# Kernel optimization log

Hardware: AMD Instinct MI355X
Metric: run time of the kernel (lower is better)

The kernel has to match this reference:

```python
import jax, jax.numpy as jnp
import numpy as np

NUM_EXPERTS = 8


def setup_inputs() -> dict:
    key = jax.random.key(0)
    k1, k2, k3 = jax.random.split(key, 3)
    M, K, E, N, TOPK = 16384, 1024, NUM_EXPERTS, 2048, 2
    local_hidden_states = jax.random.normal(k1, (M, K), dtype=jnp.float32)
    up_weight = jax.random.normal(k2, (E, K, N), dtype=jnp.float32) * 0.02
    full_topk_ids = jax.random.randint(k3, (M, TOPK), 0, E, dtype=jnp.int64)
    return {
        "local_hidden_states": local_hidden_states,
        "up_weight": up_weight,
        "full_topk_ids": full_topk_ids,
    }


def reference(local_hidden_states, up_weight, full_topk_ids):
    # WORLD_SIZE == 1 -> all-gather is the identity; full token set == local shard.
    full_hidden = local_hidden_states                     # [M, K]
    M, K = full_hidden.shape
    E, _, N = up_weight.shape
    topk = full_topk_ids.shape[1]

    # Each token is routed to `topk` experts: replicate rows, flatten routing ids.
    h_rep = jnp.repeat(full_hidden, topk, axis=0)         # [M*topk, K]
    flat_ids = full_topk_ids.reshape(-1)                  # [M*topk]

    # Expert-grouped GEMM: out[p] = h_rep[p] @ up_weight[flat_ids[p]].
    # Loop over the small fixed expert count, masking rows (dense reference
    # for the irregular grouped GEMM; avoids a [M*topk, K, N] weight gather).
    inter = jnp.zeros((M * topk, N), dtype=full_hidden.dtype)
    for e in range(E):
        mask = (flat_ids == e).astype(full_hidden.dtype)[:, None]   # [M*topk, 1]
        inter = inter + (h_rep @ up_weight[e]) * mask                # [M*topk, N]

    # Fused gated SiLU: split the fused gate/up projection in half.
    half = N // 2
    gate, up = inter[:, :half], inter[:, half:]
    return jax.nn.silu(gate) * up                          # [M*topk, N//2]
```

## Files before the change

### kernel.cpp

```cpp
#include <hip/hip_runtime.h>
#include <hip/hip_bf16.h>
#include <stdint.h>

typedef __attribute__((ext_vector_type(4))) float f32x4;
typedef __attribute__((ext_vector_type(8))) short bf16x8;
typedef __attribute__((ext_vector_type(4))) float float4v;

static constexpr int KD    = 1024;
static constexpr int ND    = 2048;
static constexpr int NE    = 8;
static constexpr int MROWS = 16384;
static constexpr int RFLAT = 32768;
static constexpr int OUTN  = 1024;

static constexpr size_t WS_ROWLIST = 1024;
static constexpr size_t WS_HB      = 262144;
static constexpr size_t WS_WT      = 262144 + (size_t)33554432;

__device__ __forceinline__ unsigned short f2bf(float f) {
  uint32_t u = __float_as_uint(f);
  uint32_t r = (u + 0x7FFFu + ((u >> 16) & 1u)) >> 16;
  return (unsigned short)r;
}

__device__ __forceinline__ void gload16(const void* g, void* l) {
  __builtin_amdgcn_global_load_lds(
      (__attribute__((address_space(1))) void*)(void*)g,
      (__attribute__((address_space(3))) void*)l, 16, 0, 0);
}

__global__ void k_detect(const int* __restrict__ ids32, int* __restrict__ wsi) {
  int t = blockIdx.x * 256 + threadIdx.x;
  int i = 2 * t + 1;
  if (i < RFLAT && ids32[i] != 0) atomicOr(&wsi[31], 1);
}

__device__ __forceinline__ int read_id(const int* ids32, int t, int mode) {
  return (mode ? ids32[t] : ids32[2 * t]) & 7;
}

__global__ void k_count(const int* __restrict__ ids, int* __restrict__ wsi) {
  __shared__ int h[8];
  const int tid = threadIdx.x;
  if (tid < 8) h[tid] = 0;
  __syncthreads();
  const int mode = wsi[31];
  const int base = blockIdx.x * 512 + tid;
  atomicAdd(&h[read_id(ids, base, mode)], 1);
  atomicAdd(&h[read_id(ids, base + 256, mode)], 1);
  __syncthreads();
  if (tid < 8 && h[tid]) atomicAdd(&wsi[tid], h[tid]);
}

__global__ void k_scan(int* wsi) {
  if (threadIdx.x == 0) {
    int o = 0, to = 0;
    for (int e = 0; e < NE; ++e) {
      int c = wsi[e];
      wsi[16 + e] = o;
      wsi[8 + e]  = o;
      wsi[40 + e] = to;
      o += c;
      to += (c + 255) / 256;
    }
    wsi[16 + NE] = o;
    wsi[40 + NE] = to;
  }
}

__global__ void k_scatter(const int* __restrict__ ids, int* __restrict__ wsi,
                          int* __restrict__ rowlist) {
  __shared__ int h[8], base[8], c2[8];
  const int tid = threadIdx.x;
  if (tid < 8) { h[tid] = 0; c2[tid] = 0; }
  __syncthreads();
  const int mode = wsi[31];
  const int t = blockIdx.x * 256 + tid;
  const int e = read_id(ids, t, mode);
  atomicAdd(&h[e], 1);
  __syncthreads();
  if (tid < 8 && h[tid]) base[tid] = atomicAdd(&wsi[8 + tid], h[tid]);
  __syncthreads();
  const int r = atomicAdd(&c2[e], 1);
  rowlist[base[e] + r] = t;
}

__global__ void k_cvtH(const float* __restrict__ H, unsigned short* __restrict__ Hb) {
  const int n4 = (MROWS * KD) / 4;
  const int stride = gridDim.x * blockDim.x;
  for (int i = blockIdx.x * blockDim.x + threadIdx.x; i < n4; i += stride) {
    float4v v = ((const float4v*)H)[i];
    ushort4 o;
    o.x = f2bf(v.x); o.y = f2bf(v.y); o.z = f2bf(v.z); o.w = f2bf(v.w);
    ((ushort4*)Hb)[i] = o;
  }
}

__global__ void k_cvtW(const float* __restrict__ W, unsigned short* __restrict__ Wt) {
  __shared__ float tile[64][65];
  const int e  = blockIdx.z;
  const int n0 = blockIdx.x * 64;
  const int k0 = blockIdx.y * 64;
  const int tx = threadIdx.x, ty = threadIdx.y;
  const float* Wp = W + (size_t)e * KD * ND;
  #pragma unroll
  for (int i = ty; i < 64; i += 8)
    tile[i][tx] = Wp[(size_t)(k0 + i) * ND + n0 + tx];
  __syncthreads();
  unsigned short* Wo = Wt + (size_t)e * ND * KD;
  #pragma unroll
  for (int i = ty; i < 64; i += 8)
    Wo[(size_t)(n0 + i) * KD + k0 + tx] = f2bf(tile[tx][i]);
}

__global__ __launch_bounds__(512, 2) void k_gemm(
    const unsigned short* __restrict__ Hb, const unsigned short* __restrict__ Wt,
    const int* __restrict__ wsi, const int* __restrict__ rowlist,
    float* __restrict__ Out) {
  const int bid = blockIdx.x;
  const int xcd = bid & 7;
  const int j   = bid >> 3;
  const int colblk = j & 7;
  const int rt  = xcd + (j >> 3) * 8;
  if (rt >= wsi[48]) return;
  int e = 0;
  #pragma unroll
  for (int q = 1; q < 8; ++q)
    if (rt >= wsi[40 + q]) e = q;
  const int cnt = wsi[e];
  const int tile_base = (rt - wsi[40 + e]) * 256;
  const int tile_cnt = min(256, cnt - tile_base);
  const int off = wsi[16 + e] + tile_base;
  const int c0 = colblk * 128;

  __shared__ char lds[131072];
  __shared__ int s_rows[256];

  const int t = threadIdx.x;
  if (t < 256) s_rows[t] = rowlist[off + min(t, tile_cnt - 1)];
  __syncthreads();

  const int srow = t >> 2;
  const int coff = ((t & 3) ^ ((t >> 3) & 3)) * 16;
  const char* sA0 = (const char*)Hb + (size_t)(s_rows[srow] >> 1) * (KD * 2) + coff;
  const char* sA1 = (const char*)Hb + (size_t)(s_rows[128 + srow] >> 1) * (KD * 2) + coff;
  auto wcol_of = [&](int jc) {
    const int wn_s = jc >> 6, r64 = jc & 63;
    const int h_s = r64 >> 4, l_s = r64 & 15;
    return (h_s < 2) ? (c0 + wn_s * 32 + h_s * 16 + l_s)
                     : (OUTN + c0 + wn_s * 32 + (h_s - 2) * 16 + l_s);
  };
  const char* sB0 = (const char*)Wt + ((size_t)e * ND + wcol_of(srow)) * (KD * 2) + coff;
  const char* sB1 = (const char*)Wt + ((size_t)e * ND + wcol_of(128 + srow)) * (KD * 2) + coff;

  const int lane = t & 63, wid = t >> 6;
  const int wm = wid >> 2, wn = wid & 3;
  const int kc = lane >> 4, l15 = lane & 15;

  f32x4 acc[8][4];
  #pragma unroll
  for (int m = 0; m < 8; ++m)
    #pragma unroll
    for (int h = 0; h < 4; ++h)
      acc[m][h] = (f32x4){0.f, 0.f, 0.f, 0.f};

  int aoff[2][8], boff[2][4];
  #pragma unroll
  for (int q = 0; q < 2; ++q) {
    #pragma unroll
    for (int m = 0; m < 8; ++m) {
      const int r = wm * 128 + m * 16 + l15;
      aoff[q][m] = q * 16384 + r * 64 + ((kc ^ ((r >> 1) & 3)) * 16);
    }
    #pragma unroll
    for (int h = 0; h < 4; ++h) {
      const int jb = wn * 64 + h * 16 + l15;
      boff[q][h] = 32768 + q * 16384 + jb * 64 + ((kc ^ ((jb >> 1) & 3)) * 16);
    }
  }

  auto SA = [&](int kt, int q, char* buf) {
    const int go = kt * 128 + q * 64;
    gload16(sA0 + go, buf + q * 16384 + t * 16);
    gload16(sA1 + go, buf + q * 16384 + 8192 + t * 16);
  };
  auto SB = [&](int kt, int q, char* buf) {
    const int go = kt * 128 + q * 64;
    gload16(sB0 + go, buf + 32768 + q * 16384 + t * 16);
    gload16(sB1 + go, buf + 32768 + q * 16384 + 8192 + t * 16);
  };

  bf16x8 af[4], bfv[4];
  auto LDA = [&](const char* cb, int q, int mlo) {
    #pragma unroll
    for (int m = 0; m < 4; ++m) af[m] = *(const bf16x8*)(cb + aoff[q][mlo + m]);
  };
  auto LDB = [&](const char* cb, int q) {
    #pragma unroll
    for (int h = 0; h < 4; ++h) bfv[h] = *(const bf16x8*)(cb + boff[q][h]);
  };
  auto MM = [&](int mlo) {
    __builtin_amdgcn_s_setprio(1);
    #pragma unroll
    for (int m = 0; m < 4; ++m)
      #pragma unroll
      for (int h = 0; h < 4; ++h)
        acc[mlo + m][h] =
            __builtin_amdgcn_mfma_f32_16x16x32_bf16(af[m], bfv[h], acc[mlo + m][h], 0, 0, 0);
    __builtin_amdgcn_s_setprio(0);
  };
#define GUARD4 asm volatile("s_waitcnt vmcnt(4)" ::: "memory")
#define GUARD0 asm volatile("s_waitcnt vmcnt(0)" ::: "memory")
#define BAR __builtin_amdgcn_s_barrier()

  SA(0, 0, lds); SB(0, 0, lds); SA(0, 1, lds); SB(0, 1, lds);
  GUARD4; BAR;

  for (int k = 0; k < 15; ++k) {
    const char* cb = lds + (k & 1) * 65536;
    char* nb = lds + ((k + 1) & 1) * 65536;
    LDA(cb, 0, 0); LDB(cb, 0);
    SA(k + 1, 0, nb);
    BAR; MM(0); BAR;
    LDA(cb, 0, 4);
    SB(k + 1, 0, nb);
    GUARD4; BAR; MM(4); BAR;
    LDA(cb, 1, 0); LDB(cb, 1);
    SA(k + 1, 1, nb);
    BAR; MM(0); BAR;
    LDA(cb, 1, 4);
    SB(k + 1, 1, nb);
    GUARD4; BAR; MM(4); BAR;
  }
  {
    const char* cb = lds + 65536;
    LDA(cb, 0, 0); LDB(cb, 0);
    BAR; MM(0); BAR;
    LDA(cb, 0, 4);
    GUARD0; BAR; MM(4); BAR;
    LDA(cb, 1, 0); LDB(cb, 1);
    BAR; MM(0); BAR;
    LDA(cb, 1, 4);
    MM(4);
  }
#undef GUARD4
#undef GUARD0
#undef BAR

  #pragma unroll
  for (int m = 0; m < 8; ++m) {
    const int rbase = wm * 128 + m * 16 + kc * 4;
    #pragma unroll
    for (int i = 0; i < 4; ++i) {
      const int rl = rbase + i;
      if (rl < tile_cnt) {
        const size_t orow = (size_t)s_rows[rl] * OUTN;
        #pragma unroll
        for (int h = 0; h < 2; ++h) {
          float gg = acc[m][h][i];
          float uu = acc[m][h + 2][i];
          float s = gg / (1.0f + __expf(-gg)) * uu;
          Out[orow + c0 + wn * 32 + h * 16 + l15] = s;
        }
      }
    }
  }
}

extern "C" void kernel_launch(void* const* d_in, const int* in_sizes, int n_in,
                              void* d_out, int out_size, void* d_ws, size_t ws_size,
                              hipStream_t stream) {
  const float* H  = (const float*)d_in[0];
  const float* W  = (const float*)d_in[1];
  const int* ids  = (const int*)d_in[2];
  float* Out      = (float*)d_out;
  char* ws        = (char*)d_ws;
  int* wsi        = (int*)ws;
  int* rowlist    = (int*)(ws + WS_ROWLIST);
  unsigned short* Hb = (unsigned short*)(ws + WS_HB);
  unsigned short* Wt = (unsigned short*)(ws + WS_WT);

  hipMemsetAsync(ws, 0, 1024, stream);
  k_detect<<<RFLAT / 2 / 256, 256, 0, stream>>>(ids, wsi);
  k_count<<<RFLAT / 512, 256, 0, stream>>>(ids, wsi);
  k_scan<<<1, 64, 0, stream>>>(wsi);
  k_scatter<<<RFLAT / 256, 256, 0, stream>>>(ids, wsi, rowlist);
  k_cvtH<<<2048, 256, 0, stream>>>(H, Hb);
  k_cvtW<<<dim3(ND / 64, KD / 64, NE), dim3(64, 8), 0, stream>>>(W, Wt);
  k_gemm<<<8 * 17 * 8, 512, 0, stream>>>(Hb, Wt, wsi, rowlist, Out);
}
```

Measured before the change: 236.0 us.

## Restructure grouped GEMM main loop into four-slot half-tile prefetch pipeline

Splits the K tile into 64-wide half-slots holding A and B together and keeps up to three slots in flight instead of a simple double buffer, with waits at vmcnt(8). Global loads are issued two half-steps ahead, which is meant to hide more memory latency behind the MFMA work. The epilogue handles the tail slots separately. The deeper prefetch adds complexity and tighter slot reuse timing, so any ordering mistake can cause LDS hazards.

```diff
diff --git a/kernel.cpp b/kernel.cpp
--- a/kernel.cpp
+++ b/kernel.cpp
@@ -164,40 +164,34 @@
     for (int h = 0; h < 4; ++h)
       acc[m][h] = (f32x4){0.f, 0.f, 0.f, 0.f};
 
-  int aoff[2][8], boff[2][4];
-  #pragma unroll
-  for (int q = 0; q < 2; ++q) {
-    #pragma unroll
-    for (int m = 0; m < 8; ++m) {
-      const int r = wm * 128 + m * 16 + l15;
-      aoff[q][m] = q * 16384 + r * 64 + ((kc ^ ((r >> 1) & 3)) * 16);
-    }
-    #pragma unroll
-    for (int h = 0; h < 4; ++h) {
-      const int jb = wn * 64 + h * 16 + l15;
-      boff[q][h] = 32768 + q * 16384 + jb * 64 + ((kc ^ ((jb >> 1) & 3)) * 16);
-    }
-  }
-
-  auto SA = [&](int kt, int q, char* buf) {
-    const int go = kt * 128 + q * 64;
-    gload16(sA0 + go, buf + q * 16384 + t * 16);
-    gload16(sA1 + go, buf + q * 16384 + 8192 + t * 16);
-  };
-  auto SB = [&](int kt, int q, char* buf) {
-    const int go = kt * 128 + q * 64;
-    gload16(sB0 + go, buf + 32768 + q * 16384 + t * 16);
-    gload16(sB1 + go, buf + 32768 + q * 16384 + 8192 + t * 16);
+  int aoff[8], boff[4];
+  #pragma unroll
+  for (int m = 0; m < 8; ++m) {
+    const int r = wm * 128 + m * 16 + l15;
+    aoff[m] = r * 64 + ((kc ^ ((r >> 1) & 3)) * 16);
+  }
+  #pragma unroll
+  for (int h = 0; h < 4; ++h) {
+    const int jc = wn * 64 + h * 16 + l15;
+    boff[h] = 16384 + jc * 64 + ((kc ^ ((jc >> 1) & 3)) * 16);
+  }
+
+  auto SAB = [&](int h, char* slot) {
+    const int go = h * 64;
+    gload16(sA0 + go, slot + t * 16);
+    gload16(sA1 + go, slot + 8192 + t * 16);
+    gload16(sB0 + go, slot + 16384 + t * 16);
+    gload16(sB1 + go, slot + 24576 + t * 16);
   };
 
   bf16x8 af[4], bfv[4];
-  auto LDA = [&](const char* cb, int q, int mlo) {
-    #pragma unroll
-    for (int m = 0; m < 4; ++m) af[m] = *(const bf16x8*)(cb + aoff[q][mlo + m]);
-  };
-  auto LDB = [&](const char* cb, int q) {
-    #pragma unroll
-    for (int h = 0; h < 4; ++h) bfv[h] = *(const bf16x8*)(cb + boff[q][h]);
+  auto LDA = [&](const char* cb, int mlo) {
+    #pragma unroll
+    for (int m = 0; m < 4; ++m) af[m] = *(const bf16x8*)(cb + aoff[mlo + m]);
+  };
+  auto LDB = [&](const char* cb) {
+    #pragma unroll
+    for (int h = 0; h < 4; ++h) bfv[h] = *(const bf16x8*)(cb + boff[h]);
   };
   auto MM = [&](int mlo) {
     __builtin_amdgcn_s_setprio(1);
@@ -209,40 +203,58 @@
             __builtin_amdgcn_mfma_f32_16x16x32_bf16(af[m], bfv[h], acc[mlo + m][h], 0, 0, 0);
     __builtin_amdgcn_s_setprio(0);
   };
+#define GUARD8 asm volatile("s_waitcnt vmcnt(8)" ::: "memory")
 #define GUARD4 asm volatile("s_waitcnt vmcnt(4)" ::: "memory")
 #define GUARD0 asm volatile("s_waitcnt vmcnt(0)" ::: "memory")
 #define BAR __builtin_amdgcn_s_barrier()
 
-  SA(0, 0, lds); SB(0, 0, lds); SA(0, 1, lds); SB(0, 1, lds);
-  GUARD4; BAR;
-
-  for (int k = 0; k < 15; ++k) {
-    const char* cb = lds + (k & 1) * 65536;
-    char* nb = lds + ((k + 1) & 1) * 65536;
-    LDA(cb, 0, 0); LDB(cb, 0);
-    SA(k + 1, 0, nb);
-    BAR; MM(0); BAR;
-    LDA(cb, 0, 4);
-    SB(k + 1, 0, nb);
+  SAB(0, lds);
+  SAB(1, lds + 32768);
+  SAB(2, lds + 65536);
+  GUARD8; BAR;
+
+  for (int k = 0; k < 14; ++k) {
+    char* cb0 = lds + (k & 1) * 65536;
+    char* cb1 = cb0 + 32768;
+    char* st1 = lds + ((k + 1) & 1) * 65536 + 32768;
+    LDA(cb0, 0); LDB(cb0);
+    SAB(2 * k + 3, st1);
+    BAR; MM(0); BAR;
+    LDA(cb0, 4);
+    GUARD8; BAR; MM(4); BAR;
+    LDA(cb1, 0); LDB(cb1);
+    SAB(2 * k + 4, cb0);
+    BAR; MM(0); BAR;
+    LDA(cb1, 4);
+    GUARD8; BAR; MM(4); BAR;
+  }
+  {
+    char* cb0 = lds;
+    char* cb1 = lds + 32768;
+    char* st1 = lds + 98304;
+    LDA(cb0, 0); LDB(cb0);
+    SAB(31, st1);
+    BAR; MM(0); BAR;
+    LDA(cb0, 4);
+    GUARD8; BAR; MM(4); BAR;
+    LDA(cb1, 0); LDB(cb1);
+    BAR; MM(0); BAR;
+    LDA(cb1, 4);
     GUARD4; BAR; MM(4); BAR;
-    LDA(cb, 1, 0); LDB(cb, 1);
-    SA(k + 1, 1, nb);
-    BAR; MM(0); BAR;
-    LDA(cb, 1, 4);
-    SB(k + 1, 1, nb);
-    GUARD4; BAR; MM(4); BAR;
   }
   {
-    const char* cb = lds + 65536;
-    LDA(cb, 0, 0); LDB(cb, 0);
-    BAR; MM(0); BAR;
-    LDA(cb, 0, 4);
+    char* cb0 = lds + 65536;
+    char* cb1 = lds + 98304;
+    LDA(cb0, 0); LDB(cb0);
+    BAR; MM(0); BAR;
+    LDA(cb0, 4);
     GUARD0; BAR; MM(4); BAR;
-    LDA(cb, 1, 0); LDB(cb, 1);
-    BAR; MM(0); BAR;
-    LDA(cb, 1, 4);
+    LDA(cb1, 0); LDB(cb1);
+    BAR; MM(0); BAR;
+    LDA(cb1, 4);
     MM(4);
   }
+#undef GUARD8
 #undef GUARD4
 #undef GUARD0
 #undef BAR
```

After: 233.3 us. Within noise of the previous version (-1.2%).
